# Optimization experiments

Hardware: AMD Instinct MI355X
Metric: run time of the kernel (lower is better)

The kernel has to match this reference:

```python
import jax, jax.numpy as jnp
import numpy as np

DIM = 384
NUM_HEADS = 8
HEAD_DIM = DIM // NUM_HEADS
SCALE = HEAD_DIM ** -0.5
MLP_HIDDEN = int(DIM * 4.0)
EPS = 1e-6


def setup_inputs() -> dict:
    key = jax.random.key(0)
    ks = jax.random.split(key, 8)
    s = 0.02
    return {
        "x": jax.random.normal(ks[0], (2, DIM, 8, 16, 16), dtype=jnp.float32),
        "g1": jnp.ones((DIM,), jnp.float32),
        "b1": jnp.zeros((DIM,), jnp.float32),
        "Wqkv": jax.random.normal(ks[1], (DIM, 3 * DIM), jnp.float32) * s,  # no bias (qkv_bias=False)
        "Wo": jax.random.normal(ks[2], (DIM, DIM), jnp.float32) * s,
        "bo": jnp.zeros((DIM,), jnp.float32),
        "g2": jnp.ones((DIM,), jnp.float32),
        "b2": jnp.zeros((DIM,), jnp.float32),
        "W1": jax.random.normal(ks[3], (DIM, MLP_HIDDEN), jnp.float32) * s,
        "b1m": jnp.zeros((MLP_HIDDEN,), jnp.float32),
        "W2": jax.random.normal(ks[4], (MLP_HIDDEN, DIM), jnp.float32) * s,
        "b2m": jnp.zeros((DIM,), jnp.float32),
    }


def _layernorm(x, g, b):
    mu = jnp.mean(x, axis=-1, keepdims=True)
    var = jnp.mean(jnp.square(x - mu), axis=-1, keepdims=True)
    return (x - mu) * jax.lax.rsqrt(var + EPS) * g + b


def _attention(h, Wqkv, Wo, bo):
    B, N, C = h.shape
    qkv = h @ Wqkv  # [B, N, 3C]
    qkv = qkv.reshape(B, N, 3, NUM_HEADS, HEAD_DIM).transpose(2, 0, 3, 1, 4)
    q, k, v = qkv[0], qkv[1], qkv[2]  # each [B, H, N, d]
    att = jax.nn.softmax(jnp.einsum('bhxd,bhyd->bhxy', q, k) * SCALE, axis=-1)
    out = jnp.einsum('bhxy,bhyd->bhxd', att, v)  # [B, H, N, d]
    out = out.transpose(0, 2, 1, 3).reshape(B, N, C)
    return out @ Wo + bo


def reference(x, g1, b1, Wqkv, Wo, bo, g2, b2, W1, b1m, W2, b2m):
    B, C, D, H, W = x.shape
    h = x.transpose(0, 2, 3, 4, 1).reshape(B, D * H * W, C)  # b (d h w) c
    h = h + _attention(_layernorm(h, g1, b1), Wqkv, Wo, bo)
    m = _layernorm(h, g2, b2)
    m = jax.nn.gelu(m @ W1 + b1m, approximate=False) @ W2 + b2m
    h = h + m
    return h.reshape(B, D, H, W, C).transpose(0, 4, 1, 2, 3)
```

## Files before the change

kernel.cpp:

```cpp
#include <hip/hip_runtime.h>
#include <hip/hip_bf16.h>
#include <math.h>

#define DIM    384
#define NHEAD  8
#define HDIM   48
#define NTOK   2048
#define BATCH  2
#define TOKS   (BATCH * NTOK)
#define HIDDEN 1536

typedef __bf16 bf16x8 __attribute__((ext_vector_type(8)));
typedef float  f32x4  __attribute__((ext_vector_type(4)));
typedef unsigned short u16;

union bfu { __hip_bfloat16 h; u16 u; };

__device__ __forceinline__ void load_lds16(const void* g, void* l) {
    __builtin_amdgcn_global_load_lds(
        (const __attribute__((address_space(1))) void*)g,
        (__attribute__((address_space(3))) void*)l, 16, 0, 0);
}

__global__ __launch_bounds__(256) void prep(
    const float* __restrict__ Wqkv, __hip_bfloat16* __restrict__ WqkvT,
    const float* __restrict__ x, const float* __restrict__ g,
    const float* __restrict__ bta,
    float* __restrict__ hOut, __hip_bfloat16* __restrict__ y) {
    __shared__ __align__(16) char smem[384 * 33 * 4];
    int id = blockIdx.x;
    int tid = threadIdx.x;
    if (id < 432) {
        float (*t)[33] = (float(*)[33])smem;
        const int R = 384, C = 1152, tc = C / 32;
        int i0 = (id / tc) * 32, j0 = (id % tc) * 32;
        int tx = tid & 31, ty = tid >> 5;
#pragma unroll
        for (int k = 0; k < 32; k += 8)
            t[ty + k][tx] = Wqkv[(size_t)(i0 + ty + k) * C + j0 + tx];
        __syncthreads();
#pragma unroll
        for (int k = 0; k < 32; k += 8)
            WqkvT[(size_t)(j0 + ty + k) * R + i0 + tx] = __float2bfloat16(t[tx][ty + k]);
    } else {
        float* t = (float*)smem;
        int id2 = id - 432;
        int n0 = (id2 & 63) * 32, b = id2 >> 6;
        const float* xb = x + (size_t)b * DIM * NTOK;
        for (int idx = tid; idx < 384 * 32; idx += 256) {
            int c = idx >> 5, n = idx & 31;
            t[c * 33 + n] = xb[(size_t)c * NTOK + n0 + n];
        }
        __syncthreads();
        int wid = tid >> 6, lane = tid & 63;
#pragma unroll
        for (int it = 0; it < 8; ++it) {
            int tl = it * 4 + wid;
            float v[6];
            float s = 0.f;
#pragma unroll
            for (int i = 0; i < 6; ++i) { v[i] = t[(lane + 64 * i) * 33 + tl]; s += v[i]; }
#pragma unroll
            for (int o = 32; o; o >>= 1) s += __shfl_xor(s, o, 64);
            float mu = s * (1.f / DIM);
            float s2 = 0.f;
#pragma unroll
            for (int i = 0; i < 6; ++i) { float d = v[i] - mu; s2 += d * d; }
#pragma unroll
            for (int o = 32; o; o >>= 1) s2 += __shfl_xor(s2, o, 64);
            float r = rsqrtf(s2 * (1.f / DIM) + 1e-6f);
            size_t tok = (size_t)b * NTOK + n0 + tl;
#pragma unroll
            for (int i = 0; i < 6; ++i) {
                int c = lane + 64 * i;
                hOut[tok * DIM + c] = v[i];
                y[tok * DIM + c] = __float2bfloat16((v[i] - mu) * r * g[c] + bta[c]);
            }
        }
    }
}

__global__ __launch_bounds__(256) void qkv_gemm_xpose(
    const __hip_bfloat16* __restrict__ A,
    const __hip_bfloat16* __restrict__ BT,
    __hip_bfloat16* __restrict__ Cout,
    __hip_bfloat16* __restrict__ vtout,
    const float* __restrict__ Wo, const float* __restrict__ W1,
    const float* __restrict__ W2,
    __hip_bfloat16* __restrict__ WoT, __hip_bfloat16* __restrict__ W1T,
    __hip_bfloat16* __restrict__ W2T) {
    __shared__ __align__(16) u16 As[2][64 * 32];
    __shared__ __align__(16) u16 Bs[2][64 * 32];
    const int lid = blockIdx.x;
    const int tid = threadIdx.x;
    if (lid < 1152) {
        const int swz = (lid & 7) * 144 + (lid >> 3);
        const int bx = swz % 18, by = swz / 18;
        const int bm = by * 64, bn = bx * 64;
        const int K = DIM;
        int w = tid >> 6, l = tid & 63;
        int m0 = (w >> 1) * 32, n0 = (w & 1) * 32;
        int lm = l & 15, ksel = l >> 4;

        int row = tid >> 2, c16 = tid & 3;
        const __hip_bfloat16* ga = A  + (size_t)(bm + row) * K + c16 * 8;
        const __hip_bfloat16* gb = BT + (size_t)(bn + row) * K + c16 * 8;

        f32x4 acc[2][2] = {};
        for (int k0 = 0; k0 < K; k0 += 64) {
#pragma unroll
            for (int c = 0; c < 2; ++c) {
                load_lds16(ga + k0 + c * 32, &As[c][tid * 8]);
                load_lds16(gb + k0 + c * 32, &Bs[c][tid * 8]);
            }
            __syncthreads();
#pragma unroll
            for (int kk = 0; kk < 2; ++kk) {
                bf16x8 af0 = *(const bf16x8*)&As[kk][(m0 +      lm) * 32 + ksel * 8];
                bf16x8 af1 = *(const bf16x8*)&As[kk][(m0 + 16 + lm) * 32 + ksel * 8];
                bf16x8 bf0 = *(const bf16x8*)&Bs[kk][(n0 +      lm) * 32 + ksel * 8];
                bf16x8 bf1 = *(const bf16x8*)&Bs[kk][(n0 + 16 + lm) * 32 + ksel * 8];
                acc[0][0] = __builtin_amdgcn_mfma_f32_16x16x32_bf16(af0, bf0, acc[0][0], 0, 0, 0);
                acc[0][1] = __builtin_amdgcn_mfma_f32_16x16x32_bf16(af0, bf1, acc[0][1], 0, 0, 0);
                acc[1][0] = __builtin_amdgcn_mfma_f32_16x16x32_bf16(af1, bf0, acc[1][0], 0, 0, 0);
                acc[1][1] = __builtin_amdgcn_mfma_f32_16x16x32_bf16(af1, bf1, acc[1][1], 0, 0, 0);
            }
            __syncthreads();
        }
#pragma unroll
        for (int i = 0; i < 2; ++i)
#pragma unroll
            for (int j = 0; j < 2; ++j)
#pragma unroll
                for (int r = 0; r < 4; ++r) {
                    int rg = bm + m0 + i * 16 + ksel * 4 + r;
                    int cg = bn + n0 + j * 16 + lm;
                    float v = acc[i][j][r];
                    if (cg < 768) {
                        Cout[(size_t)rg * 1152 + cg] = __float2bfloat16(v);
                    } else {
                        int c = cg - 768, hh = c / 48, dd = c - hh * 48;
                        int bb = rg >> 11, n = rg & (NTOK - 1);
                        int kk = n & 127;
                        int pos = ((kk >> 6) << 6) + ((kk & 15) << 2) + ((kk >> 4) & 3);
                        vtout[((size_t)(bb * NHEAD + hh) * 48 + dd) * 2048
                              + (n & ~127) + pos] = __float2bfloat16(v);
                    }
                }
    } else {
        float (*t)[33] = (float(*)[33])As;
        int id = lid - 1152;
        const float* src; __hip_bfloat16* dst; int R, C;
        if (id < 144)      {            src = Wo; dst = WoT; R = 384;  C = 384; }
        else if (id < 720) { id -= 144; src = W1; dst = W1T; R = 384;  C = 1536; }
        else               { id -= 720; src = W2; dst = W2T; R = 1536; C = 384; }
        int tc = C / 32;
        int i0 = (id / tc) * 32, j0 = (id % tc) * 32;
        int tx = tid & 31, ty = tid >> 5;
#pragma unroll
        for (int k = 0; k < 32; k += 8)
            t[ty + k][tx] = src[(size_t)(i0 + ty + k) * C + j0 + tx];
        __syncthreads();
#pragma unroll
        for (int k = 0; k < 32; k += 8)
            dst[(size_t)(j0 + ty + k) * R + i0 + tx] = __float2bfloat16(t[tx][ty + k]);
    }
}

template<int BK, bool GELU>
__global__ __launch_bounds__(256) void gemm_mfma(
    const __hip_bfloat16* __restrict__ A,
    const __hip_bfloat16* __restrict__ BT,
    const float* __restrict__ bias,
    __hip_bfloat16* __restrict__ Cout,
    int M, int N, int K) {
    constexpr int NC = BK / 32;
    __shared__ __align__(16) u16 As[NC][64 * 32];
    __shared__ __align__(16) u16 Bs[NC][64 * 32];
    const int nwg = gridDim.x * gridDim.y;
    const int lid = blockIdx.y * gridDim.x + blockIdx.x;
    const int swz = (lid & 7) * (nwg >> 3) + (lid >> 3);
    const int bx = swz % gridDim.x, by = swz / gridDim.x;
    int bm = by * 64, bn = bx * 64;
    int tid = threadIdx.x;
    int w = tid >> 6, l = tid & 63;
    int m0 = (w >> 1) * 32, n0 = (w & 1) * 32;
    int lm = l & 15, ksel = l >> 4;

    int row = tid >> 2, c16 = tid & 3;
    const __hip_bfloat16* ga = A  + (size_t)(bm + row) * K + c16 * 8;
    const __hip_bfloat16* gb = BT + (size_t)(bn + row) * K + c16 * 8;

    f32x4 acc[2][2] = {};
    for (int k0 = 0; k0 < K; k0 += BK) {
#pragma unroll
        for (int c = 0; c < NC; ++c) {
            load_lds16(ga + k0 + c * 32, &As[c][tid * 8]);
            load_lds16(gb + k0 + c * 32, &Bs[c][tid * 8]);
        }
        __syncthreads();
#pragma unroll
        for (int kk = 0; kk < NC; ++kk) {
            bf16x8 af0 = *(const bf16x8*)&As[kk][(m0 +      lm) * 32 + ksel * 8];
            bf16x8 af1 = *(const bf16x8*)&As[kk][(m0 + 16 + lm) * 32 + ksel * 8];
            bf16x8 bf0 = *(const bf16x8*)&Bs[kk][(n0 +      lm) * 32 + ksel * 8];
            bf16x8 bf1 = *(const bf16x8*)&Bs[kk][(n0 + 16 + lm) * 32 + ksel * 8];
            acc[0][0] = __builtin_amdgcn_mfma_f32_16x16x32_bf16(af0, bf0, acc[0][0], 0, 0, 0);
            acc[0][1] = __builtin_amdgcn_mfma_f32_16x16x32_bf16(af0, bf1, acc[0][1], 0, 0, 0);
            acc[1][0] = __builtin_amdgcn_mfma_f32_16x16x32_bf16(af1, bf0, acc[1][0], 0, 0, 0);
            acc[1][1] = __builtin_amdgcn_mfma_f32_16x16x32_bf16(af1, bf1, acc[1][1], 0, 0, 0);
        }
        __syncthreads();
    }

#pragma unroll
    for (int i = 0; i < 2; ++i)
#pragma unroll
        for (int j = 0; j < 2; ++j)
#pragma unroll
            for (int r = 0; r < 4; ++r) {
                int rg = bm + m0 + i * 16 + ksel * 4 + r;
                int cg = bn + n0 + j * 16 + lm;
                float v = acc[i][j][r];
                if (bias) v += bias[cg];
                if (GELU) v = 0.5f * v * (1.f + erff(v * 0.7071067811865475f));
                Cout[(size_t)rg * N + cg] = __float2bfloat16(v);
            }
}

__global__ __launch_bounds__(256) void w2_gemm(
    const __hip_bfloat16* __restrict__ A,
    const __hip_bfloat16* __restrict__ BT,
    const float* __restrict__ bias,
    const float* __restrict__ res,
    float* __restrict__ outp) {
    __shared__ __align__(16) u16 As[32 * 128];
    __shared__ __align__(16) u16 Bs[64 * 128];
    __shared__ float ct[32 * 65];
    const int K = HIDDEN, N = DIM;
    const int nwg = gridDim.x * gridDim.y;
    const int lid = blockIdx.y * gridDim.x + blockIdx.x;
    const int swz = (lid & 7) * (nwg >> 3) + (lid >> 3);
    const int bx = swz % gridDim.x, by = swz / gridDim.x;
    const int bm = by * 32, bn = bx * 64;
    const int tid = threadIdx.x;
    const int w = tid >> 6, l = tid & 63;
    const int n0 = w * 16;
    const int lm = l & 15, ksel = l >> 4;
    const int xr = lm & 7;

    f32x4 acc[2] = {};
    for (int k0 = 0; k0 < K; k0 += 128) {
#pragma unroll
        for (int i = 0; i < 2; ++i) {
            int idx = tid + i * 256;
            int row = idx >> 4, p = idx & 15;
            int g = p ^ (row & 7);
            load_lds16(A + (size_t)(bm + row) * K + k0 + g * 8, (char*)As + idx * 16);
        }
#pragma unroll
        for (int i = 0; i < 4; ++i) {
            int idx = tid + i * 256;
            int row = idx >> 4, p = idx & 15;
            int g = p ^ (row & 7);
            load_lds16(BT + (size_t)(bn + row) * K + k0 + g * 8, (char*)Bs + idx * 16);
        }
        __syncthreads();
#pragma unroll
        for (int kk = 0; kk < 4; ++kk) {
            int gq = ((kk * 4 + ksel) ^ xr) * 8;
            bf16x8 af0 = *(const bf16x8*)&As[lm        * 128 + gq];
            bf16x8 af1 = *(const bf16x8*)&As[(16 + lm) * 128 + gq];
            bf16x8 bf  = *(const bf16x8*)&Bs[(n0 + lm) * 128 + gq];
            acc[0] = __builtin_amdgcn_mfma_f32_16x16x32_bf16(af0, bf, acc[0], 0, 0, 0);
            acc[1] = __builtin_amdgcn_mfma_f32_16x16x32_bf16(af1, bf, acc[1], 0, 0, 0);
        }
        __syncthreads();
    }

#pragma unroll
    for (int m = 0; m < 2; ++m)
#pragma unroll
        for (int r = 0; r < 4; ++r) {
            int ml = m * 16 + ksel * 4 + r;
            int cl = n0 + lm;
            float v = acc[m][r] + bias[bn + cl]
                    + res[(size_t)(bm + ml) * N + bn + cl];
            ct[ml * 65 + cl] = v;
        }
    __syncthreads();
    int bb = bm >> 11, nb = bm & (NTOK - 1);
    float* op = outp + (size_t)bb * DIM * NTOK + nb;
#pragma unroll
    for (int cc = w * 2; cc < 64; cc += 8) {
        int cl = cc + (l >> 5), rw = l & 31;
        op[(size_t)(bn + cl) * NTOK + rw] = ct[rw * 65 + cl];
    }
}

__global__ __launch_bounds__(256) void wo_ln(
    const __hip_bfloat16* __restrict__ A,
    const __hip_bfloat16* __restrict__ BT,
    const float* __restrict__ bo,
    const float* __restrict__ g2, const float* __restrict__ b2,
    float* __restrict__ h,
    __hip_bfloat16* __restrict__ y) {
    __shared__ __align__(16) u16 As[16 * 64];
    __shared__ __align__(16) u16 Bs[384 * 64];
    __shared__ float red[16 * 8];
    const int r0 = blockIdx.x * 16;
    const int tid = threadIdx.x;
    const int w = tid >> 6, l = tid & 63, lm = l & 15, quad = l >> 4;

    const int arow = tid >> 3;
    const int ag = (tid & 7) ^ (arow & 7);
    const __hip_bfloat16* gaA = A + (size_t)(r0 + arow) * DIM + ag * 8;
    const int xr = lm & 7;

    f32x4 acc[6] = {};
    for (int k0 = 0; k0 < DIM; k0 += 64) {
        if (tid < 128) load_lds16(gaA + k0, (char*)As + tid * 16);
#pragma unroll
        for (int i = 0; i < 12; ++i) {
            int idx = tid + i * 256;
            int brow = idx >> 3;
            int bg = (idx & 7) ^ (brow & 7);
            load_lds16(BT + (size_t)brow * DIM + k0 + bg * 8, (char*)Bs + idx * 16);
        }
        __syncthreads();
#pragma unroll
        for (int kk = 0; kk < 2; ++kk) {
            int goff = ((kk * 4 + quad) ^ xr) * 8;
            bf16x8 af = *(const bf16x8*)&As[lm * 64 + goff];
#pragma unroll
            for (int n = 0; n < 6; ++n) {
                bf16x8 bf = *(const bf16x8*)&Bs[(w * 96 + n * 16 + lm) * 64 + goff];
                acc[n] = __builtin_amdgcn_mfma_f32_16x16x32_bf16(af, bf, acc[n], 0, 0, 0);
            }
        }
        __syncthreads();
    }

    float vv[6][4];
    float s1[4] = {0.f, 0.f, 0.f, 0.f}, s2[4] = {0.f, 0.f, 0.f, 0.f};
#pragma unroll
    for (int r = 0; r < 4; ++r) {
        int rg = r0 + quad * 4 + r;
#pragma unroll
        for (int n = 0; n < 6; ++n) {
            int cg = w * 96 + n * 16 + lm;
            float v = acc[n][r] + bo[cg] + h[(size_t)rg * DIM + cg];
            vv[n][r] = v;
            s1[r] += v;
            s2[r] += v * v;
            h[(size_t)rg * DIM + cg] = v;
        }
    }
#pragma unroll
    for (int r = 0; r < 4; ++r) {
#pragma unroll
        for (int o = 8; o; o >>= 1) {
            s1[r] += __shfl_xor(s1[r], o, 64);
            s2[r] += __shfl_xor(s2[r], o, 64);
        }
        if (lm == 0) {
            red[(quad * 4 + r) * 8 + w * 2]     = s1[r];
            red[(quad * 4 + r) * 8 + w * 2 + 1] = s2[r];
        }
    }
    __syncthreads();
#pragma unroll
    for (int r = 0; r < 4; ++r) {
        int lr = quad * 4 + r;
        float S1 = red[lr * 8] + red[lr * 8 + 2] + red[lr * 8 + 4] + red[lr * 8 + 6];
        float S2 = red[lr * 8 + 1] + red[lr * 8 + 3] + red[lr * 8 + 5] + red[lr * 8 + 7];
        float mu = S1 * (1.f / DIM);
        float var = S2 * (1.f / DIM) - mu * mu;
        float rstd = rsqrtf(var + 1e-6f);
        int rg = r0 + lr;
#pragma unroll
        for (int n = 0; n < 6; ++n) {
            int cg = w * 96 + n * 16 + lm;
            y[(size_t)rg * DIM + cg] =
                __float2bfloat16((vv[n][r] - mu) * rstd * g2[cg] + b2[cg]);
        }
    }
}

#define ATK 128
#define PSTR 136
__global__ __launch_bounds__(512, 4) void attn_mfma(
    const u16* __restrict__ qkv,
    const u16* __restrict__ vt,
    __hip_bfloat16* __restrict__ outp) {
    __shared__ __align__(16) u16 PQ[64 * PSTR];
    __shared__ __align__(16) u16 Ks[128 * 72];
    __shared__ __align__(16) u16 Vs[48 * PSTR];
    const int lid = (blockIdx.z * NHEAD + blockIdx.y) * (NTOK / 64) + blockIdx.x;
    const int swz = (lid & 7) * 64 + (lid >> 3);
    const int q0 = (swz & 31) * 64;
    const int h = (swz >> 5) & 7, b = swz >> 8;
    const int tid = threadIdx.x;
    const int w = tid >> 6, l = tid & 63, lm = l & 15, quad = l >> 4;
    const int qc = w >> 1, kh = w & 1;

    for (int idx = tid; idx < 128; idx += 512) {
        int r = idx >> 1, c = idx & 1;
        *(uint4*)&PQ[r * 72 + 48 + c * 8] = uint4{0, 0, 0, 0};
    }
    for (int idx = tid; idx < 256; idx += 512) {
        int r = idx >> 1, c = idx & 1;
        *(uint4*)&Ks[r * 72 + 48 + c * 8] = uint4{0, 0, 0, 0};
    }
    const u16* qbase = qkv + (size_t)(b * NTOK + q0) * 1152 + h * 48;
    for (int idx = tid; idx < 384; idx += 512) {
        int r = idx / 6, c = idx % 6;
        *(uint4*)&PQ[r * 72 + c * 8] = *(const uint4*)(qbase + (size_t)r * 1152 + c * 8);
    }
    __syncthreads();

    bf16x8 aq0 = *(const bf16x8*)&PQ[(qc * 16 + lm) * 72 +  0 + quad * 8];
    bf16x8 aq1 = *(const bf16x8*)&PQ[(qc * 16 + lm) * 72 + 32 + quad * 8];

    float l_i[4] = {0.f, 0.f, 0.f, 0.f};
    f32x4 o_acc[3] = {};

    const u16* kbase = qkv + (size_t)(b * NTOK) * 1152 + 384 + h * 48;
    const u16* vbase = vt + (size_t)(b * NHEAD + h) * 48 * 2048;
    const float sc2 = 0.14433756729740643f * 1.4426950408889634f;

    const int kr0 = tid / 6,  kc0 = tid % 6;
    const int kr1 = (tid + 512) / 6, kc1 = (tid + 512) % 6;
    const int vd0 = tid >> 4, vc0 = tid & 15;
    const int vd1 = (tid + 512) >> 4, vc1 = (tid + 512) & 15;
    const bool two = tid < 256;
    uint4 kp0, kp1, vp0, vp1;

    {
        kp0 = *(const uint4*)(kbase + (size_t)kr0 * 1152 + kc0 * 8);
        vp0 = *(const uint4*)(vbase + (size_t)vd0 * 2048 + vc0 * 8);
        if (two) {
            kp1 = *(const uint4*)(kbase + (size_t)kr1 * 1152 + kc1 * 8);
            vp1 = *(const uint4*)(vbase + (size_t)vd1 * 2048 + vc1 * 8);
        }
    }

    for (int kt = 0; kt < NTOK / ATK; ++kt) {
        __syncthreads();
        *(uint4*)&Ks[kr0 * 72 + kc0 * 8] = kp0;
        *(uint4*)&Vs[vd0 * PSTR + vc0 * 8] = vp0;
        if (two) {
            *(uint4*)&Ks[kr1 * 72 + kc1 * 8] = kp1;
            *(uint4*)&Vs[vd1 * PSTR + vc1 * 8] = vp1;
        }
        __syncthreads();
        if (kt + 1 < NTOK / ATK) {
            const u16* kb = kbase + (size_t)(kt + 1) * ATK * 1152;
            const u16* vb = vbase + (size_t)(kt + 1) * ATK;
            kp0 = *(const uint4*)(kb + (size_t)kr0 * 1152 + kc0 * 8);
            vp0 = *(const uint4*)(vb + (size_t)vd0 * 2048 + vc0 * 8);
            if (two) {
                kp1 = *(const uint4*)(kb + (size_t)kr1 * 1152 + kc1 * 8);
                vp1 = *(const uint4*)(vb + (size_t)vd1 * 2048 + vc1 * 8);
            }
        }

        f32x4 s[4];
#pragma unroll
        for (int ntp = 0; ntp < 4; ++ntp) {
            int nt = kh * 4 + ntp;
            bf16x8 kf0 = *(const bf16x8*)&Ks[(nt * 16 + lm) * 72 +  0 + quad * 8];
            bf16x8 kf1 = *(const bf16x8*)&Ks[(nt * 16 + lm) * 72 + 32 + quad * 8];
            f32x4 t = {};
            t = __builtin_amdgcn_mfma_f32_16x16x32_bf16(aq0, kf0, t, 0, 0, 0);
            t = __builtin_amdgcn_mfma_f32_16x16x32_bf16(aq1, kf1, t, 0, 0, 0);
            s[ntp] = t;
        }

#pragma unroll
        for (int r = 0; r < 4; ++r) {
            u16 pr[4];
#pragma unroll
            for (int ntp = 0; ntp < 4; ++ntp) {
                float p = exp2f(s[ntp][r] * sc2);
                l_i[r] += p;
                bfu cv; cv.h = __float2bfloat16(p);
                pr[ntp] = cv.u;
            }
            *(uint2*)&PQ[(qc * 16 + quad * 4 + r) * PSTR + kh * 64 + lm * 4] =
                *(const uint2*)pr;
        }

#pragma unroll
        for (int ksp = 0; ksp < 2; ++ksp) {
            int ks = kh * 2 + ksp;
            bf16x8 pf = *(const bf16x8*)&PQ[(qc * 16 + lm) * PSTR + ks * 32 + quad * 8];
#pragma unroll
            for (int nt = 0; nt < 3; ++nt) {
                bf16x8 vf = *(const bf16x8*)&Vs[(nt * 16 + lm) * PSTR + ks * 32 + quad * 8];
                o_acc[nt] = __builtin_amdgcn_mfma_f32_16x16x32_bf16(pf, vf, o_acc[nt], 0, 0, 0);
            }
        }
    }

    __syncthreads();
    float* red = (float*)Ks;
    if (kh == 1) {
        f32x4* base = (f32x4*)&red[(qc * 64 + l) * 16];
        base[0] = o_acc[0]; base[1] = o_acc[1]; base[2] = o_acc[2];
        f32x4 lv; lv[0] = l_i[0]; lv[1] = l_i[1]; lv[2] = l_i[2]; lv[3] = l_i[3];
        base[3] = lv;
    }
    __syncthreads();
    if (kh == 0) {
        f32x4* base = (f32x4*)&red[(qc * 64 + l) * 16];
        o_acc[0] += base[0]; o_acc[1] += base[1]; o_acc[2] += base[2];
        f32x4 lv = base[3];
#pragma unroll
        for (int r = 0; r < 4; ++r) {
            float lsum = l_i[r] + lv[r];
#pragma unroll
            for (int o = 8; o; o >>= 1) lsum += __shfl_xor(lsum, o, 64);
            float inv = 1.f / lsum;
#pragma unroll
            for (int nt = 0; nt < 3; ++nt)
                outp[(size_t)(b * NTOK + q0 + qc * 16 + quad * 4 + r) * DIM
                     + h * 48 + nt * 16 + lm]
                    = __float2bfloat16(o_acc[nt][r] * inv);
        }
    }
}

extern "C" void kernel_launch(void* const* d_in, const int* in_sizes, int n_in,
                              void* d_out, int out_size, void* d_ws, size_t ws_size,
                              hipStream_t stream) {
    const float* x    = (const float*)d_in[0];
    const float* g1   = (const float*)d_in[1];
    const float* b1   = (const float*)d_in[2];
    const float* Wqkv = (const float*)d_in[3];
    const float* Wo   = (const float*)d_in[4];
    const float* bo   = (const float*)d_in[5];
    const float* g2   = (const float*)d_in[6];
    const float* b2   = (const float*)d_in[7];
    const float* W1   = (const float*)d_in[8];
    const float* b1m  = (const float*)d_in[9];
    const float* W2   = (const float*)d_in[10];
    const float* b2m  = (const float*)d_in[11];
    float* out = (float*)d_out;

    char* p = (char*)d_ws;
    float* bufH = (float*)p;                       p += (size_t)TOKS * DIM * 4;
    char* qkvp = p;
    __hip_bfloat16* bufQKVb = (__hip_bfloat16*)p;  p += (size_t)TOKS * 3 * DIM * 2;
    __hip_bfloat16* bufVT   = (__hip_bfloat16*)p;  p += (size_t)TOKS * DIM * 2;
    __hip_bfloat16* bufNb   = (__hip_bfloat16*)p;  p += (size_t)TOKS * DIM * 2;
    __hip_bfloat16* bufAb   = (__hip_bfloat16*)p;  p += (size_t)TOKS * DIM * 2;
    __hip_bfloat16* WqkvT   = (__hip_bfloat16*)p;  p += (size_t)3 * DIM * DIM * 2;
    __hip_bfloat16* WoT     = (__hip_bfloat16*)p;  p += (size_t)DIM * DIM * 2;
    __hip_bfloat16* W1T     = (__hip_bfloat16*)p;  p += (size_t)HIDDEN * DIM * 2;
    __hip_bfloat16* W2T     = (__hip_bfloat16*)p;  p += (size_t)DIM * HIDDEN * 2;
    __hip_bfloat16* bufHIDb = (__hip_bfloat16*)qkvp;

    prep<<<432 + 128, 256, 0, stream>>>(Wqkv, WqkvT, x, g1, b1, bufH, bufNb);
    qkv_gemm_xpose<<<1152 + 1296, 256, 0, stream>>>(
        bufNb, WqkvT, bufQKVb, bufVT, Wo, W1, W2, WoT, W1T, W2T);
    attn_mfma<<<dim3(NTOK / 64, NHEAD, BATCH), 512, 0, stream>>>(
        (const u16*)bufQKVb, (const u16*)bufVT, bufAb);
    wo_ln<<<TOKS / 16, 256, 0, stream>>>(bufAb, WoT, bo, g2, b2, bufH, bufNb);
    gemm_mfma<64, true><<<dim3(HIDDEN / 64, TOKS / 64), 256, 0, stream>>>(
        bufNb, W1T, b1m, bufHIDb, TOKS, HIDDEN, DIM);
    w2_gemm<<<dim3(DIM / 64, TOKS / 32), 256, 0, stream>>>(
        bufHIDb, W2T, b2m, bufH, out);
}
```

Before: 179.6 us.

## Double attention query tile to 128 rows with 1024-thread blocks sharing K/V tiles

```diff
diff --git a/kernel.cpp b/kernel.cpp
--- a/kernel.cpp
+++ b/kernel.cpp
@@ -389,80 +389,76 @@
 
 #define ATK 128
 #define PSTR 136
-__global__ __launch_bounds__(512, 4) void attn_mfma(
+__global__ __launch_bounds__(1024, 4) void attn_mfma(
     const u16* __restrict__ qkv,
     const u16* __restrict__ vt,
     __hip_bfloat16* __restrict__ outp) {
-    __shared__ __align__(16) u16 PQ[64 * PSTR];
+    __shared__ __align__(16) u16 PQ[128 * PSTR];
     __shared__ __align__(16) u16 Ks[128 * 72];
     __shared__ __align__(16) u16 Vs[48 * PSTR];
-    const int lid = (blockIdx.z * NHEAD + blockIdx.y) * (NTOK / 64) + blockIdx.x;
-    const int swz = (lid & 7) * 64 + (lid >> 3);
-    const int q0 = (swz & 31) * 64;
-    const int h = (swz >> 5) & 7, b = swz >> 8;
+    const int lid = (blockIdx.z * NHEAD + blockIdx.y) * (NTOK / 128) + blockIdx.x;
+    const int swz = (lid & 7) * 32 + (lid >> 3);
+    const int q0 = (swz & 15) * 128;
+    const int h = (swz >> 4) & 7, b = swz >> 7;
     const int tid = threadIdx.x;
     const int w = tid >> 6, l = tid & 63, lm = l & 15, quad = l >> 4;
     const int qc = w >> 1, kh = w & 1;
 
-    for (int idx = tid; idx < 128; idx += 512) {
-        int r = idx >> 1, c = idx & 1;
+    if (tid < 256) {
+        int r = tid >> 1, c = tid & 1;
         *(uint4*)&PQ[r * 72 + 48 + c * 8] = uint4{0, 0, 0, 0};
-    }
-    for (int idx = tid; idx < 256; idx += 512) {
-        int r = idx >> 1, c = idx & 1;
+    } else if (tid < 512) {
+        int t2 = tid - 256;
+        int r = t2 >> 1, c = t2 & 1;
         *(uint4*)&Ks[r * 72 + 48 + c * 8] = uint4{0, 0, 0, 0};
     }
     const u16* qbase = qkv + (size_t)(b * NTOK + q0) * 1152 + h * 48;
-    for (int idx = tid; idx < 384; idx += 512) {
-        int r = idx / 6, c = idx % 6;
+    if (tid < 768) {
+        int r = tid / 6, c = tid % 6;
         *(uint4*)&PQ[r * 72 + c * 8] = *(const uint4*)(qbase + (size_t)r * 1152 + c * 8);
     }
-    __syncthreads();
-
-    bf16x8 aq0 = *(const bf16x8*)&PQ[(qc * 16 + lm) * 72 +  0 + quad * 8];
-    bf16x8 aq1 = *(const bf16x8*)&PQ[(qc * 16 + lm) * 72 + 32 + quad * 8];
-
-    float l_i[4] = {0.f, 0.f, 0.f, 0.f};
-    f32x4 o_acc[3] = {};
 
     const u16* kbase = qkv + (size_t)(b * NTOK) * 1152 + 384 + h * 48;
     const u16* vbase = vt + (size_t)(b * NHEAD + h) * 48 * 2048;
     const float sc2 = 0.14433756729740643f * 1.4426950408889634f;
 
-    const int kr0 = tid / 6,  kc0 = tid % 6;
-    const int kr1 = (tid + 512) / 6, kc1 = (tid + 512) % 6;
-    const int vd0 = tid >> 4, vc0 = tid & 15;
-    const int vd1 = (tid + 512) >> 4, vc1 = (tid + 512) & 15;
-    const bool two = tid < 256;
-    uint4 kp0, kp1, vp0, vp1;
-
-    {
-        kp0 = *(const uint4*)(kbase + (size_t)kr0 * 1152 + kc0 * 8);
-        vp0 = *(const uint4*)(vbase + (size_t)vd0 * 2048 + vc0 * 8);
-        if (two) {
-            kp1 = *(const uint4*)(kbase + (size_t)kr1 * 1152 + kc1 * 8);
-            vp1 = *(const uint4*)(vbase + (size_t)vd1 * 2048 + vc1 * 8);
-        }
-    }
+    const bool isK0 = tid < 768;
+    const int kr0 = tid / 6, kc0 = tid % 6;
+    const int j0v = tid - 768;
+    const int vd0 = j0v >> 4, vc0 = j0v & 15;
+    const bool two = tid < 512;
+    const int j1v = tid + 256;
+    const int vd1 = j1v >> 4, vc1 = j1v & 15;
+    uint4 p0, p1;
+
+    if (isK0) p0 = *(const uint4*)(kbase + (size_t)kr0 * 1152 + kc0 * 8);
+    else      p0 = *(const uint4*)(vbase + (size_t)vd0 * 2048 + vc0 * 8);
+    if (two)  p1 = *(const uint4*)(vbase + (size_t)vd1 * 2048 + vc1 * 8);
+    if (isK0) *(uint4*)&Ks[kr0 * 72 + kc0 * 8] = p0;
+    else      *(uint4*)&Vs[vd0 * PSTR + vc0 * 8] = p0;
+    if (two)  *(uint4*)&Vs[vd1 * PSTR + vc1 * 8] = p1;
+    __syncthreads();
+
+    bf16x8 aq0 = *(const bf16x8*)&PQ[(qc * 16 + lm) * 72 +  0 + quad * 8];
+    bf16x8 aq1 = *(const bf16x8*)&PQ[(qc * 16 + lm) * 72 + 32 + quad * 8];
+
+    float l_i[4] = {0.f, 0.f, 0.f, 0.f};
+    f32x4 o_acc[3] = {};
 
     for (int kt = 0; kt < NTOK / ATK; ++kt) {
         __syncthreads();
-        *(uint4*)&Ks[kr0 * 72 + kc0 * 8] = kp0;
-        *(uint4*)&Vs[vd0 * PSTR + vc0 * 8] = vp0;
-        if (two) {
-            *(uint4*)&Ks[kr1 * 72 + kc1 * 8] = kp1;
-            *(uint4*)&Vs[vd1 * PSTR + vc1 * 8] = vp1;
-        }
-        __syncthreads();
+        if (kt > 0) {
+            if (isK0) *(uint4*)&Ks[kr0 * 72 + kc0 * 8] = p0;
+            else      *(uint4*)&Vs[vd0 * PSTR + vc0 * 8] = p0;
+            if (two)  *(uint4*)&Vs[vd1 * PSTR + vc1 * 8] = p1;
+            __syncthreads();
+        }
         if (kt + 1 < NTOK / ATK) {
             const u16* kb = kbase + (size_t)(kt + 1) * ATK * 1152;
             const u16* vb = vbase + (size_t)(kt + 1) * ATK;
-            kp0 = *(const uint4*)(kb + (size_t)kr0 * 1152 + kc0 * 8);
-            vp0 = *(const uint4*)(vb + (size_t)vd0 * 2048 + vc0 * 8);
-            if (two) {
-                kp1 = *(const uint4*)(kb + (size_t)kr1 * 1152 + kc1 * 8);
-                vp1 = *(const uint4*)(vb + (size_t)vd1 * 2048 + vc1 * 8);
-            }
+            if (isK0) p0 = *(const uint4*)(kb + (size_t)kr0 * 1152 + kc0 * 8);
+            else      p0 = *(const uint4*)(vb + (size_t)vd0 * 2048 + vc0 * 8);
+            if (two)  p1 = *(const uint4*)(vb + (size_t)vd1 * 2048 + vc1 * 8);
         }
 
         f32x4 s[4];
@@ -504,7 +500,7 @@
     }
 
     __syncthreads();
-    float* red = (float*)Ks;
+    float* red = (float*)PQ;
     if (kh == 1) {
         f32x4* base = (f32x4*)&red[(qc * 64 + l) * 16];
         base[0] = o_acc[0]; base[1] = o_acc[1]; base[2] = o_acc[2];
@@ -564,7 +560,7 @@
     prep<<<432 + 128, 256, 0, stream>>>(Wqkv, WqkvT, x, g1, b1, bufH, bufNb);
     qkv_gemm_xpose<<<1152 + 1296, 256, 0, stream>>>(
         bufNb, WqkvT, bufQKVb, bufVT, Wo, W1, W2, WoT, W1T, W2T);
-    attn_mfma<<<dim3(NTOK / 64, NHEAD, BATCH), 512, 0, stream>>>(
+    attn_mfma<<<dim3(NTOK / 128, NHEAD, BATCH), 1024, 0, stream>>>(
         (const u16*)bufQKVb, (const u16*)bufVT, bufAb);
     wo_ln<<<TOKS / 16, 256, 0, stream>>>(bufAb, WoT, bo, g2, b2, bufH, bufNb);
     gemm_mfma<64, true><<<dim3(HIDDEN / 64, TOKS / 64), 256, 0, stream>>>(
```

Measured after the change: 180.2 us. About the same (+0.3%).
